# Performance work log

Measured on AMD Instinct MI355X. Metric: run time of the kernel, lower is better.

The kernel has to match this reference:

```python
import jax, jax.numpy as jnp
import numpy as np

N_NODE = 50000
D = 64
N_HEADS = 8
N_LAYERS = 2
NEG = -1e9
PAD = 0
STDV = 1.0 / np.sqrt(D)


def _l2norm(x, axis):
    n = jnp.sqrt(jnp.sum(x * x, axis=axis, keepdims=True))
    return x / jnp.maximum(n, 1e-12)


def _hgconv(x, theta, bias, edge_index):
    # PyG HypergraphConv (use_attention=False): out = D^-1 H B^-1 H^T (x @ theta) + bias
    xt = x @ theta
    node, hedge = edge_index[0], edge_index[1]
    ones = jnp.ones(node.shape[0], x.dtype)
    Bdeg = jax.ops.segment_sum(ones, hedge, num_segments=N_NODE)   # hyperedge degree
    Ddeg = jax.ops.segment_sum(ones, node, num_segments=N_NODE)    # node degree
    m = jax.ops.segment_sum(xt[node], hedge, num_segments=N_NODE)  # nodes -> hyperedges
    m = m * jnp.where(Bdeg > 0, 1.0 / Bdeg, 0.0)[:, None]
    out = jax.ops.segment_sum(m[hedge], node, num_segments=N_NODE) # hyperedges -> nodes
    out = out * jnp.where(Ddeg > 0, 1.0 / Ddeg, 0.0)[:, None]
    return out + bias


def _mha(x, w, pad_mask, reverse):
    # w: [4, D, D] -> q, k, v, out projections. reverse=True attends to future (triu).
    B, L, d = x.shape
    dk = d // N_HEADS
    split = lambda h: h.reshape(B, L, N_HEADS, dk).transpose(0, 2, 1, 3)
    q, k, v = split(x @ w[0]), split(x @ w[1]), split(x @ w[2])
    scores = jnp.einsum('bhid,bhjd->bhij', q, k) / jnp.sqrt(jnp.asarray(dk, x.dtype))
    tri = jnp.triu(jnp.ones((L, L), bool)) if reverse else jnp.tril(jnp.ones((L, L), bool))
    scores = jnp.where(tri[None, None], scores, NEG)
    scores = jnp.where(pad_mask[:, None, None, :], NEG, scores)
    attn = jax.nn.softmax(scores, axis=-1)
    out = jnp.einsum('bhij,bhjd->bhid', attn, v).transpose(0, 2, 1, 3).reshape(B, L, d)
    return out @ w[3], attn


def _prev_user_mask(seq):
    # scatter -1000 at every user id already seen up to position i (index 0 = PAD column)
    B, L = seq.shape
    tril = jnp.tril(jnp.ones((L, L), bool))
    idx = jnp.where(tril[None], seq[:, None, :], 0)                       # [B,L,L]
    idx = jnp.concatenate([idx, jnp.zeros((B, L, 1), idx.dtype)], axis=2)  # [B,L,L+1]
    b = jnp.arange(B)[:, None, None]
    i = jnp.arange(L)[None, :, None]
    return jnp.zeros((B, L, N_NODE), jnp.float32).at[b, i, idx].set(-1000.0)


def _hg_user(emb_table, gate_w, gate_b, att, att_m, theta, theta_b, edges):
    chans = []
    for c in range(3):
        x = emb_table * jax.nn.sigmoid(emb_table @ gate_w[c] + gate_b[c])  # self-gating
        acc, cur = x, x
        for k in range(N_LAYERS):
            cur = _hgconv(cur, theta[k], theta_b[k], edges[c])
            acc = acc + _l2norm(cur, axis=1)
        chans.append(acc / (N_LAYERS + 1))  # mean over [input, layer1, layer2]
    logits = jnp.stack([jnp.sum(att * (c @ att_m), axis=1) for c in chans], axis=1)  # [N,3]
    score = jax.nn.softmax(logits, axis=-1)
    return sum(score[:, i:i + 1] * chans[i] for i in range(3))


def setup_inputs() -> dict:
    key = jax.random.key(0)
    ks = jax.random.split(key, 20)
    u = lambda k, shp: jax.random.uniform(k, shp, jnp.float32, -STDV, STDV)
    B, L, E = 16, 50, 800000
    return {
        'input_seq': jax.random.randint(ks[0], (B, L), 0, N_NODE),
        'label_seq': jax.random.randint(ks[1], (B, L), 0, N_NODE),
        'input_time': jax.random.randint(ks[2], (B, L), 0, 100000),
        'label_time': jax.random.randint(ks[3], (B, L), 0, 100000),
        'edge_index_g': jax.random.randint(ks[4], (2, E), 0, N_NODE),
        'edge_index_i': jax.random.randint(ks[5], (2, E), 0, N_NODE),
        'edge_index_u': jax.random.randint(ks[6], (2, E), 0, N_NODE),
        'emb_table': u(ks[7], (N_NODE, D)),
        'gate_w': u(ks[8], (3, D, D)),
        'gate_b': u(ks[9], (3, D)),
        'att': u(ks[10], (D,)),
        'att_m': u(ks[11], (D, D)),
        'theta': u(ks[12], (N_LAYERS, D, D)),
        'theta_b': u(ks[13], (N_LAYERS, D)),
        'w_hist': u(ks[14], (4, D, D)),
        'w_fut': u(ks[15], (4, D, D)),
    }


def reference(input_seq, label_seq, input_time, label_time,
              edge_index_g, edge_index_i, edge_index_u,
              emb_table, gate_w, gate_b, att, att_m, theta, theta_b, w_hist, w_fut):
    # input_time / label_time are accepted but unused, as in the original forward.
    HG = _hg_user(emb_table, gate_w, gate_b, att, att_m, theta, theta_b,
                  (edge_index_g, edge_index_i, edge_index_u))
    pad_in = input_seq == PAD
    pad_lb = label_seq == PAD
    past_att_out, past_dist = _mha(HG[input_seq], w_hist, pad_in, reverse=False)
    fut_att_out, fut_dist = _mha(HG[label_seq], w_fut, pad_lb, reverse=True)
    output_past = (past_att_out @ HG.T + _prev_user_mask(input_seq)).reshape(-1, N_NODE)
    future_output = (fut_att_out @ HG.T).reshape(-1, N_NODE)
    return (output_past, future_output, past_dist, fut_dist,
            _l2norm(past_att_out, axis=1), _l2norm(fut_att_out, axis=1))
```

## Files before the change

### kernel.cpp

```cpp
#include <hip/hip_runtime.h>
#include <math.h>

#define N_NODE 50000
#define DD 64
#define NE 800000
#define BB 16
#define LL 50
#define NH 8
#define DK 8
#define NEGV -1e9f
#define NB 49
#define NBLK 256
#define EPB 3125

#define OFF_PDIST 80000000u
#define OFF_FDIST 80320000u
#define OFF_L2P 80640000u
#define OFF_L2F 80691200u

typedef unsigned short ushortt;
typedef __attribute__((ext_vector_type(8))) short bf16x8v;
typedef __attribute__((ext_vector_type(4))) float f32x4v;

__device__ __forceinline__ float b2f(ushortt h) { return __uint_as_float(((unsigned)h) << 16); }
__device__ __forceinline__ ushortt f2b(float f) {
    unsigned u = __float_as_uint(f);
    return (ushortt)((u + 0x7fffu + ((u >> 16) & 1u)) >> 16);
}
__device__ __forceinline__ void acc8(float* a, uint4 x) {
    a[0] += b2f((ushortt)(x.x)); a[1] += b2f((ushortt)(x.x >> 16));
    a[2] += b2f((ushortt)(x.y)); a[3] += b2f((ushortt)(x.y >> 16));
    a[4] += b2f((ushortt)(x.z)); a[5] += b2f((ushortt)(x.z >> 16));
    a[6] += b2f((ushortt)(x.w)); a[7] += b2f((ushortt)(x.w >> 16));
}
__device__ __forceinline__ uint4 pack8(const float* a) {
    uint4 w;
    w.x = (unsigned)f2b(a[0]) | ((unsigned)f2b(a[1]) << 16);
    w.y = (unsigned)f2b(a[2]) | ((unsigned)f2b(a[3]) << 16);
    w.z = (unsigned)f2b(a[4]) | ((unsigned)f2b(a[5]) << 16);
    w.w = (unsigned)f2b(a[6]) | ((unsigned)f2b(a[7]) << 16);
    return w;
}

__global__ void k_zero(float* p, int n) {
    int i = blockIdx.x * 256 + threadIdx.x;
    if (i < n) p[i] = 0.0f;
}

__global__ __launch_bounds__(256) void k_cnt(const int* __restrict__ eg,
                                             const int* __restrict__ ei,
                                             const int* __restrict__ eu,
                                             int* __restrict__ hist) {
    int c = blockIdx.y;
    const int* ed = (c == 0) ? eg : ((c == 1) ? ei : eu);
    int blk = blockIdx.x;
    __shared__ int lc[2 * NB];
    int tid = threadIdx.x;
    for (int j = tid; j < 2 * NB; j += 256) lc[j] = 0;
    __syncthreads();
    int e0 = blk * EPB;
    for (int i = e0 + tid; i < e0 + EPB; i += 256) {
        atomicAdd(&lc[ed[NE + i] >> 10], 1);
        atomicAdd(&lc[NB + (ed[i] >> 10)], 1);
    }
    __syncthreads();
    for (int j = tid; j < 2 * NB; j += 256) {
        int side = (j >= NB);
        int b = side ? (j - NB) : j;
        hist[(((side * 3 + c) * NB) + b) * NBLK + blk] = lc[j];
    }
}

__global__ __launch_bounds__(256) void k_scanH(int* __restrict__ hist, int* __restrict__ bb) {
    int t6 = blockIdx.x;
    int* h = hist + t6 * NB * NBLK;
    __shared__ int part[256];
    int tid = threadIdx.x;
    const int CH = (NB * NBLK) / 256;
    int base = tid * CH;
    int s = 0;
    for (int i = 0; i < CH; i++) s += h[base + i];
    part[tid] = s;
    __syncthreads();
    for (int o = 1; o < 256; o <<= 1) {
        int v = (tid >= o) ? part[tid - o] : 0;
        __syncthreads();
        part[tid] += v;
        __syncthreads();
    }
    int run = (tid == 0) ? 0 : part[tid - 1];
    for (int i = 0; i < CH; i++) {
        int idx = base + i;
        int v = h[idx];
        if ((idx & (NBLK - 1)) == 0) bb[t6 * (NB + 1) + (idx >> 8)] = run;
        h[idx] = run;
        run += v;
    }
    if (tid == 255) bb[t6 * (NB + 1) + NB] = run;
}

__global__ __launch_bounds__(256) void k_part2(const int* __restrict__ eg,
                                               const int* __restrict__ ei,
                                               const int* __restrict__ eu,
                                               const int* __restrict__ hist,
                                               unsigned* __restrict__ poolB,
                                               unsigned* __restrict__ poolD) {
    int c = blockIdx.y;
    const int* ed = (c == 0) ? eg : ((c == 1) ? ei : eu);
    int blk = blockIdx.x;
    __shared__ int curB[NB], curD[NB];
    int tid = threadIdx.x;
    for (int j = tid; j < NB; j += 256) {
        curB[j] = hist[(((0 * 3 + c) * NB) + j) * NBLK + blk];
        curD[j] = hist[(((1 * 3 + c) * NB) + j) * NBLK + blk];
    }
    __syncthreads();
    unsigned* pB = poolB + c * 800000;
    unsigned* pD = poolD + c * 800000;
    int e0 = blk * EPB;
    for (int i = e0 + tid; i < e0 + EPB; i += 256) {
        int n = ed[i], h = ed[NE + i];
        int pb = atomicAdd(&curB[h >> 10], 1);
        pB[pb] = ((unsigned)h << 16) | (unsigned)n;
        int pd = atomicAdd(&curD[n >> 10], 1);
        pD[pd] = ((unsigned)n << 16) | (unsigned)h;
    }
}

__global__ __launch_bounds__(256) void k_bucket(const unsigned* __restrict__ poolB,
                                                const unsigned* __restrict__ poolD,
                                                const int* __restrict__ bb,
                                                int* __restrict__ nbrB3, int* __restrict__ nbrD3,
                                                int* __restrict__ offB3, int* __restrict__ offD3,
                                                float* __restrict__ invB3, float* __restrict__ invD3) {
    int b = blockIdx.x, c = blockIdx.y, side = blockIdx.z;
    const unsigned* pool = (side ? poolD : poolB) + c * 800000;
    int* nbr = (side ? nbrD3 : nbrB3) + c * 800000;
    int* off = (side ? offD3 : offB3) + c * 50001;
    float* inv = (side ? invD3 : invB3) + c * 50000;
    int t6 = side * 3 + c;
    int s0 = bb[t6 * (NB + 1) + b], s1 = bb[t6 * (NB + 1) + b + 1];
    int baseSeg = b << 10;
    __shared__ int cnt[1024];
    __shared__ int ofs[1024];
    __shared__ int part[256];
    int tid = threadIdx.x;
    for (int j = tid; j < 1024; j += 256) cnt[j] = 0;
    __syncthreads();
    for (int i = s0 + tid; i < s1; i += 256)
        atomicAdd(&cnt[(pool[i] >> 16) & 1023], 1);
    __syncthreads();
    int t4 = tid * 4;
    int a0 = cnt[t4], a1 = cnt[t4 + 1], a2 = cnt[t4 + 2], a3 = cnt[t4 + 3];
    part[tid] = a0 + a1 + a2 + a3;
    __syncthreads();
    for (int o = 1; o < 256; o <<= 1) {
        int v = (tid >= o) ? part[tid - o] : 0;
        __syncthreads();
        part[tid] += v;
        __syncthreads();
    }
    int excl = (tid == 0) ? 0 : part[tid - 1];
    ofs[t4] = excl;
    ofs[t4 + 1] = excl + a0;
    ofs[t4 + 2] = excl + a0 + a1;
    ofs[t4 + 3] = excl + a0 + a1 + a2;
    __syncthreads();
    for (int ls = tid; ls < 1024; ls += 256) {
        int seg = baseSeg + ls;
        if (seg < N_NODE) {
            off[seg] = s0 + ofs[ls];
            inv[seg] = cnt[ls] ? 1.0f / (float)cnt[ls] : 0.0f;
        }
    }
    if (b == NB - 1 && tid == 0) off[N_NODE] = NE;
    __syncthreads();
    for (int i = s0 + tid; i < s1; i += 256) {
        unsigned u = pool[i];
        int ls = (u >> 16) & 1023;
        int p = atomicAdd(&ofs[ls], 1);
        nbr[s0 + p] = (int)(u & 0xFFFFu);
    }
}

__global__ __launch_bounds__(256) void k_gateX(const float* __restrict__ emb,
                                               const float* __restrict__ gate_w,
                                               const float* __restrict__ gate_b,
                                               float* __restrict__ acc3,
                                               ushortt* __restrict__ xt3) {
    int c = blockIdx.y;
    const float* W = gate_w + c * 4096;
    const float* bias = gate_b + c * 64;
    float* acc = acc3 + (size_t)c * 3200000;
    ushortt* xt = xt3 + (size_t)c * 3200000;
    __shared__ float sW[64 * 64];
    __shared__ float sx[4][64];
    int tid = threadIdx.x;
    for (int i = tid; i < 4096; i += 256) sW[i] = W[i];
    int r = tid >> 6;
    int d = tid & 63;
    int n = blockIdx.x * 4 + r;
    sx[r][d] = emb[n * DD + d];
    __syncthreads();
    float a = bias[d];
#pragma unroll
    for (int k = 0; k < 64; k++) a += sx[r][k] * sW[k * 64 + d];
    float x = sx[r][d] * (1.0f / (1.0f + expf(-a)));
    acc[n * DD + d] = x;
    xt[n * DD + d] = f2b(x);
}

__global__ __launch_bounds__(256) void k_gathB3(const ushortt* __restrict__ xt3,
                                                const int* __restrict__ offB3,
                                                const int* __restrict__ nbrB3,
                                                const float* __restrict__ invB3,
                                                ushortt* __restrict__ m3) {
    int c = blockIdx.y;
    const ushortt* src = xt3 + (size_t)c * 3200000;
    const int* off = offB3 + c * 50001;
    const int* nbr = nbrB3 + c * 800000;
    const float* invSeg = invB3 + c * 50000;
    ushortt* dst = m3 + (size_t)c * 3200000;
    int seg = blockIdx.x * 4 + (threadIdx.x >> 6);
    int lane = threadIdx.x & 63;
    int sub = lane >> 3;
    int c8 = lane & 7;
    int s = off[seg], e = off[seg + 1];
    float a[8] = {0.f, 0.f, 0.f, 0.f, 0.f, 0.f, 0.f, 0.f};
    int i = s + sub;
    if (i < e) {
        uint4 x = ((const uint4*)(src + (size_t)nbr[i] * DD))[c8];
        for (i += 8; i < e; i += 8) {
            uint4 nx = ((const uint4*)(src + (size_t)nbr[i] * DD))[c8];
            acc8(a, x);
            x = nx;
        }
        acc8(a, x);
    }
#pragma unroll
    for (int j = 0; j < 8; j++) {
        a[j] += __shfl_xor(a[j], 8, 64);
        a[j] += __shfl_xor(a[j], 16, 64);
        a[j] += __shfl_xor(a[j], 32, 64);
    }
    if (sub == 0) {
        float sc = invSeg[seg];
        float b[8];
#pragma unroll
        for (int j = 0; j < 8; j++) b[j] = a[j] * sc;
        ((uint4*)(dst + (size_t)seg * DD))[c8] = pack8(b);
    }
}

template <int WRITE_XT>
__global__ __launch_bounds__(256) void k_gathD3f(const ushortt* __restrict__ m3,
                                                 const int* __restrict__ offD3,
                                                 const int* __restrict__ nbrD3,
                                                 const float* __restrict__ invD3,
                                                 const float* __restrict__ theta,
                                                 const float* __restrict__ theta_b,
                                                 float* __restrict__ acc3,
                                                 ushortt* __restrict__ xt3) {
    int c = blockIdx.y;
    const ushortt* m = m3 + (size_t)c * 3200000;
    const int* off = offD3 + c * 50001;
    const int* nbr = nbrD3 + c * 800000;
    const float* invD = invD3 + c * 50000;
    float* acc = acc3 + (size_t)c * 3200000;
    ushortt* xt = xt3 + (size_t)c * 3200000;

    __shared__ float sTh[64 * 64];
    __shared__ float sx[4][64];
    __shared__ float sb[64];
    int tid = threadIdx.x;
    for (int i = tid; i < 4096; i += 256) sTh[i] = theta[i];
    if (tid < 64) sb[tid] = theta_b[tid];

    int w = tid >> 6;
    int seg = blockIdx.x * 4 + w;
    int lane = tid & 63;
    int sub = lane >> 3;
    int c8 = lane & 7;
    int s = off[seg], e = off[seg + 1];
    float a[8] = {0.f, 0.f, 0.f, 0.f, 0.f, 0.f, 0.f, 0.f};
    int i = s + sub;
    if (i < e) {
        uint4 x = ((const uint4*)(m + (size_t)nbr[i] * DD))[c8];
        for (i += 8; i < e; i += 8) {
            uint4 nx = ((const uint4*)(m + (size_t)nbr[i] * DD))[c8];
            acc8(a, x);
            x = nx;
        }
        acc8(a, x);
    }
#pragma unroll
    for (int j = 0; j < 8; j++) {
        a[j] += __shfl_xor(a[j], 8, 64);
        a[j] += __shfl_xor(a[j], 16, 64);
        a[j] += __shfl_xor(a[j], 32, 64);
    }
    if (sub == 0) {
        float iD = invD[seg];
#pragma unroll
        for (int j = 0; j < 8; j++) sx[w][c8 * 8 + j] = a[j] * iD;
    }
    __syncthreads();

    int d = lane;
    float v = sb[d];
#pragma unroll
    for (int k = 0; k < 64; k++) v += sx[w][k] * sTh[k * 64 + d];
    float ss = v * v;
#pragma unroll
    for (int o = 32; o; o >>= 1) ss += __shfl_xor(ss, o, 64);
    float nr = fmaxf(sqrtf(ss), 1e-12f);
    size_t idx = (size_t)seg * DD + d;
    acc[idx] += v / nr;
    if (WRITE_XT) xt[idx] = f2b(v);
}

__global__ __launch_bounds__(256) void k_comb(const float* __restrict__ a0,
                                              const float* __restrict__ a1,
                                              const float* __restrict__ a2,
                                              const float* __restrict__ att_m,
                                              const float* __restrict__ att,
                                              float* __restrict__ HG,
                                              ushortt* __restrict__ HG16) {
    __shared__ float svv[64];
    int tid = threadIdx.x;
    if (tid < 64) {
        float s = 0.f;
        for (int k = 0; k < 64; k++) s += att_m[tid * 64 + k] * att[k];
        svv[tid] = s;
    }
    __syncthreads();
    int r = tid >> 6;
    int d = tid & 63;
    int n = blockIdx.x * 4 + r;
    float x0 = a0[n * DD + d], x1 = a1[n * DD + d], x2 = a2[n * DD + d];
    float vd = svv[d];
    float l0 = x0 * vd, l1 = x1 * vd, l2 = x2 * vd;
#pragma unroll
    for (int o = 32; o; o >>= 1) {
        l0 += __shfl_xor(l0, o, 64);
        l1 += __shfl_xor(l1, o, 64);
        l2 += __shfl_xor(l2, o, 64);
    }
    l0 *= (1.0f / 3.0f); l1 *= (1.0f / 3.0f); l2 *= (1.0f / 3.0f);
    float mx = fmaxf(l0, fmaxf(l1, l2));
    float e0 = expf(l0 - mx), e1 = expf(l1 - mx), e2 = expf(l2 - mx);
    float inv = 1.0f / (e0 + e1 + e2);
    float hv = (e0 * x0 + e1 * x1 + e2 * x2) * inv * (1.0f / 3.0f);
    HG[n * DD + d] = hv;
    HG16[n * DD + d] = f2b(hv);
}

__global__ __launch_bounds__(256) void k_attn(const float* __restrict__ HG,
                                              const int* __restrict__ iseq,
                                              const int* __restrict__ lseq,
                                              const float* __restrict__ w_hist,
                                              const float* __restrict__ w_fut,
                                              float* __restrict__ dout,
                                              ushortt* __restrict__ attout16,
                                              float* __restrict__ attoutF) {
    int b = blockIdx.x;
    int dir = blockIdx.y;
    const int* seq = (dir == 0) ? iseq : lseq;
    const float* W = (dir == 0) ? w_hist : w_fut;
    float* dist = dout + ((dir == 0) ? OFF_PDIST : OFF_FDIST);

    __shared__ float sX[LL * 64];
    __shared__ float sQ[LL * 64];
    __shared__ float sK[LL * 64];
    __shared__ float sV[LL * 64];
    __shared__ float sS[LL * LL];
    __shared__ float sInv[64];
    __shared__ int sseq[LL];

    int tid = threadIdx.x;
    int w = tid >> 6;
    int lane = tid & 63;
    if (tid < LL) sseq[tid] = seq[b * LL + tid];
    __syncthreads();
    for (int idx = tid; idx < LL * 64; idx += 256) {
        int i = idx >> 6, d = idx & 63;
        sX[idx] = HG[sseq[i] * DD + d];
    }
    __syncthreads();
    for (int idx = tid; idx < LL * 64; idx += 256) {
        int i = idx >> 6, d = idx & 63;
        float q = 0, k = 0, v = 0;
        for (int kk = 0; kk < 64; kk++) {
            float x = sX[i * 64 + kk];
            q += x * W[kk * 64 + d];
            k += x * W[4096 + kk * 64 + d];
            v += x * W[8192 + kk * 64 + d];
        }
        sQ[idx] = q; sK[idx] = k; sV[idx] = v;
    }
    __syncthreads();
    for (int idx = tid; idx < LL * 64; idx += 256) sX[idx] = 0.0f;
    __syncthreads();

    const float scale = 0.35355339059327373f;
    for (int h = 0; h < NH; h++) {
        for (int idx = tid; idx < LL * LL; idx += 256) {
            int i = idx / LL, j = idx % LL;
            float s = 0;
#pragma unroll
            for (int d = 0; d < DK; d++) s += sQ[i * 64 + h * 8 + d] * sK[j * 64 + h * 8 + d];
            s *= scale;
            bool allowed = (dir == 0) ? (j <= i) : (j >= i);
            if (!allowed) s = NEGV;
            if (sseq[j] == 0) s = NEGV;
            sS[idx] = s;
        }
        __syncthreads();
        for (int i = w; i < LL; i += 4) {
            float v = (lane < LL) ? sS[i * LL + lane] : -INFINITY;
            float mx = v;
#pragma unroll
            for (int o = 32; o; o >>= 1) mx = fmaxf(mx, __shfl_xor(mx, o, 64));
            float e = (lane < LL) ? expf(v - mx) : 0.0f;
            float sum = e;
#pragma unroll
            for (int o = 32; o; o >>= 1) sum += __shfl_xor(sum, o, 64);
            float p = e / sum;
            if (lane < LL) {
                sS[i * LL + lane] = p;
                dist[((b * NH + h) * LL + i) * LL + lane] = p;
            }
        }
        __syncthreads();
        for (int idx = tid; idx < LL * DK; idx += 256) {
            int i = idx / DK, d8 = idx % DK;
            float o = 0;
            for (int j = 0; j < LL; j++) o += sS[i * LL + j] * sV[j * 64 + h * 8 + d8];
            sX[i * 64 + h * 8 + d8] = o;
        }
        __syncthreads();
    }
    for (int idx = tid; idx < LL * 64; idx += 256) {
        int i = idx >> 6, d = idx & 63;
        float o = 0;
        for (int kk = 0; kk < 64; kk++) o += sX[i * 64 + kk] * W[3 * 4096 + kk * 64 + d];
        sQ[idx] = o;
        int row = dir * 800 + b * LL + i;
        attout16[row * 64 + d] = f2b(o);
        if (attoutF) attoutF[row * 64 + d] = o;
    }
    __syncthreads();
    if (tid < 64) {
        float s = 0;
        for (int l = 0; l < LL; l++) {
            float x = sQ[l * 64 + tid];
            s += x * x;
        }
        sInv[tid] = 1.0f / fmaxf(sqrtf(s), 1e-12f);
    }
    __syncthreads();
    float* ol2 = dout + ((dir == 0) ? OFF_L2P : OFF_L2F) + b * LL * 64;
    for (int idx = tid; idx < LL * 64; idx += 256) {
        int d = idx & 63;
        ol2[idx] = sQ[idx] * sInv[d];
    }
}

__global__ __launch_bounds__(256) void k_bigmm_mfma(const ushortt* __restrict__ A16,
                                                    const ushortt* __restrict__ HG16,
                                                    float* __restrict__ out) {
    __shared__ float sO[16][260];
    int tid = threadIdx.x;
    int lane = tid & 63;
    int w = tid >> 6;
    int rt = blockIdx.y;
    int colBase = blockIdx.x * 256;
    int lrow = lane & 15;
    int kb = (lane >> 4) * 8;
    int arow = rt * 16 + lrow;
    bf16x8v a0 = *(const bf16x8v*)(A16 + (size_t)arow * 64 + kb);
    bf16x8v a1 = *(const bf16x8v*)(A16 + (size_t)arow * 64 + kb + 32);
#pragma unroll
    for (int ct = 0; ct < 4; ct++) {
        int lc = w * 64 + ct * 16 + lrow;
        int col = colBase + lc;
        int colc = (col < N_NODE) ? col : 0;
        bf16x8v b0 = *(const bf16x8v*)(HG16 + (size_t)colc * 64 + kb);
        bf16x8v b1 = *(const bf16x8v*)(HG16 + (size_t)colc * 64 + kb + 32);
        f32x4v acc = {0.f, 0.f, 0.f, 0.f};
        acc = __builtin_amdgcn_mfma_f32_16x16x32_bf16(a0, b0, acc, 0, 0, 0);
        acc = __builtin_amdgcn_mfma_f32_16x16x32_bf16(a1, b1, acc, 0, 0, 0);
        int r0 = (lane >> 4) * 4;
#pragma unroll
        for (int j = 0; j < 4; j++) sO[r0 + j][lc] = acc[j];
    }
    __syncthreads();
#pragma unroll
    for (int j = 0; j < 4; j++) {
        int r = w * 4 + j;
        int row = rt * 16 + r;
        int c0 = colBase + lane * 4;
        f32x4v v = {sO[r][lane * 4], sO[r][lane * 4 + 1],
                    sO[r][lane * 4 + 2], sO[r][lane * 4 + 3]};
        if (c0 + 3 < N_NODE) {
            __builtin_nontemporal_store(v, (f32x4v*)(out + (size_t)row * 50000 + c0));
        } else {
            for (int t = 0; t < 4; t++)
                if (c0 + t < N_NODE) out[(size_t)row * 50000 + c0 + t] = v[t];
        }
    }
}

__global__ __launch_bounds__(64) void k_mask(const int* __restrict__ iseq,
                                             float* __restrict__ out) {
    int row = blockIdx.x;
    int b = row / LL, i = row % LL;
    __shared__ int s[LL];
    int tid = threadIdx.x;
    if (tid < LL) s[tid] = iseq[b * LL + tid];
    __syncthreads();
    float* o = out + (size_t)row * 50000;
    if (tid == 0) o[0] -= 1000.0f;
    if (tid < LL && tid <= i) {
        int c = s[tid];
        if (c > 0 && c < N_NODE) {
            bool first = true;
            for (int j = 0; j < tid; j++)
                if (s[j] == c) { first = false; break; }
            if (first) o[c] -= 1000.0f;
        }
    }
}

__global__ void k_deg(const int* __restrict__ node, const int* __restrict__ hedge,
                      float* __restrict__ Ddeg, float* __restrict__ Bdeg) {
    int e = blockIdx.x * 256 + threadIdx.x;
    if (e < NE) {
        atomicAdd(&Ddeg[node[e]], 1.0f);
        atomicAdd(&Bdeg[hedge[e]], 1.0f);
    }
}

__global__ void k_inv(float* a, int n) {
    int i = blockIdx.x * 256 + threadIdx.x;
    if (i < n) a[i] = (a[i] > 0.0f) ? (1.0f / a[i]) : 0.0f;
}

__global__ __launch_bounds__(256) void k_scat(const float* __restrict__ src,
                                              const int* __restrict__ gidx,
                                              const int* __restrict__ sidx,
                                              const float* __restrict__ scale,
                                              float* __restrict__ dst) {
    int e = blockIdx.x * 4 + (threadIdx.x >> 6);
    int d = threadIdx.x & 63;
    if (e >= NE) return;
    int g = gidx[e];
    int s = sidx[e];
    float v = src[g * DD + d];
    if (scale) v *= scale[g];
    atomicAdd(&dst[s * DD + d], v);
}

__global__ __launch_bounds__(256) void k_fin(float* __restrict__ cur,
                                             const float* __restrict__ invD,
                                             const float* __restrict__ bias,
                                             float* __restrict__ acc) {
    int r = threadIdx.x >> 6;
    int d = threadIdx.x & 63;
    int n = blockIdx.x * 4 + r;
    float v = cur[n * DD + d] * invD[n] + bias[d];
    cur[n * DD + d] = v;
    float s = v * v;
#pragma unroll
    for (int o = 32; o; o >>= 1) s += __shfl_xor(s, o, 64);
    float nr = fmaxf(sqrtf(s), 1e-12f);
    acc[n * DD + d] += v / nr;
}

__global__ __launch_bounds__(256) void k_gate(const float* __restrict__ emb,
                                              const float* __restrict__ W,
                                              const float* __restrict__ bias,
                                              float* __restrict__ cur,
                                              float* __restrict__ acc) {
    __shared__ float sW[64 * 64];
    __shared__ float sx[4][64];
    int tid = threadIdx.x;
    for (int i = tid; i < 4096; i += 256) sW[i] = W[i];
    int r = tid >> 6;
    int d = tid & 63;
    int n = blockIdx.x * 4 + r;
    sx[r][d] = emb[n * DD + d];
    __syncthreads();
    float a = bias[d];
#pragma unroll
    for (int k = 0; k < 64; k++) a += sx[r][k] * sW[k * 64 + d];
    float x = sx[r][d] * (1.0f / (1.0f + expf(-a)));
    cur[n * DD + d] = x;
    acc[n * DD + d] = x;
}

__global__ __launch_bounds__(256) void k_mm64(const float* __restrict__ X,
                                              const float* __restrict__ W,
                                              float* __restrict__ Y) {
    __shared__ float sW[64 * 64];
    __shared__ float sx[4][64];
    int tid = threadIdx.x;
    for (int i = tid; i < 4096; i += 256) sW[i] = W[i];
    int r = tid >> 6;
    int d = tid & 63;
    int n = blockIdx.x * 4 + r;
    sx[r][d] = X[n * DD + d];
    __syncthreads();
    float a = 0.0f;
#pragma unroll
    for (int k = 0; k < 64; k++) a += sx[r][k] * sW[k * 64 + d];
    Y[n * DD + d] = a;
}

__global__ __launch_bounds__(256) void k_bigmm5(const float* __restrict__ A,
                                                const float* __restrict__ HG,
                                                float* __restrict__ out) {
    int col = blockIdx.x * 256 + threadIdx.x;
    int r0 = blockIdx.y * 400;
    bool ok = (col < N_NODE);
    float4 h[16];
    const float4* hp = (const float4*)(HG + (size_t)(ok ? col : 0) * 64);
#pragma unroll
    for (int t = 0; t < 16; t++) h[t] = hp[t];
    if (!ok) return;
    for (int r = 0; r < 400; r++) {
        int row = r0 + r;
        const float* ar = A + (size_t)row * 64;
        float q0 = 0.f, q1 = 0.f, q2 = 0.f, q3 = 0.f;
#pragma unroll
        for (int t = 0; t < 16; t++) {
            q0 += ar[4 * t + 0] * h[t].x;
            q1 += ar[4 * t + 1] * h[t].y;
            q2 += ar[4 * t + 2] * h[t].z;
            q3 += ar[4 * t + 3] * h[t].w;
        }
        out[(size_t)row * 50000 + col] = (q0 + q1) + (q2 + q3);
    }
}

extern "C" void kernel_launch(void* const* d_in, const int* in_sizes, int n_in,
                              void* d_out, int out_size, void* d_ws, size_t ws_size,
                              hipStream_t stream) {
    const int* input_seq = (const int*)d_in[0];
    const int* label_seq = (const int*)d_in[1];
    const int* eg = (const int*)d_in[4];
    const int* ei = (const int*)d_in[5];
    const int* eu = (const int*)d_in[6];
    const float* emb = (const float*)d_in[7];
    const float* gate_w = (const float*)d_in[8];
    const float* gate_b = (const float*)d_in[9];
    const float* att = (const float*)d_in[10];
    const float* att_m = (const float*)d_in[11];
    const float* theta = (const float*)d_in[12];
    const float* theta_b = (const float*)d_in[13];
    const float* w_hist = (const float*)d_in[14];
    const float* w_fut = (const float*)d_in[15];

    float* out = (float*)d_out;
    float* ws = (float*)d_ws;

    const size_t HGF = 3200000;
    const int HISTN = 6 * NB * NBLK;
    const size_t needA = (HGF + 150000 + 150000 +
                          (size_t)(HISTN + 6 * (NB + 1) + 64) +
                          300006 + 4 * 2400000 +
                          2 * 2400000 +
                          3 * HGF +
                          HGF / 2 + 51200 + 1024) * 4;

    if (ws_size >= needA) {
        size_t o = 0;
        float* HG = ws + o; o += HGF;
        float* invB3 = ws + o; o += 150000;
        float* invD3 = ws + o; o += 150000;
        int* hist = (int*)(ws + o); o += HISTN;
        int* bbarr = (int*)(ws + o); o += 6 * (NB + 1) + 64;
        int* offB3 = (int*)(ws + o); o += 150003;
        int* offD3 = (int*)(ws + o); o += 150003 + 2;
        int* nbrB3 = (int*)(ws + o); o += 2400000;
        int* nbrD3 = (int*)(ws + o); o += 2400000;
        unsigned* poolB = (unsigned*)(ws + o); o += 2400000;
        unsigned* poolD = (unsigned*)(ws + o); o += 2400000;
        ushortt* xt3 = (ushortt*)(ws + o); o += 4800000;
        ushortt* m3 = (ushortt*)(ws + o); o += 4800000;
        float* acc3 = ws + o; o += 3 * HGF;
        ushortt* HG16 = (ushortt*)(ws + o); o += HGF / 2;
        ushortt* A16 = (ushortt*)(ws + o); o += 51200;

        dim3 pg(NBLK, 3);
        k_cnt<<<pg, 256, 0, stream>>>(eg, ei, eu, hist);
        k_scanH<<<6, 256, 0, stream>>>(hist, bbarr);
        k_part2<<<pg, 256, 0, stream>>>(eg, ei, eu, hist, poolB, poolD);
        dim3 dg(NB, 3, 2);
        k_bucket<<<dg, 256, 0, stream>>>(poolB, poolD, bbarr, nbrB3, nbrD3,
                                         offB3, offD3, invB3, invD3);

        dim3 ng3(12500, 3);
        k_gateX<<<ng3, 256, 0, stream>>>(emb, gate_w, gate_b, acc3, xt3);
        k_gathB3<<<ng3, 256, 0, stream>>>(xt3, offB3, nbrB3, invB3, m3);
        k_gathD3f<1><<<ng3, 256, 0, stream>>>(m3, offD3, nbrD3, invD3,
                                              theta, theta_b, acc3, xt3);
        k_gathB3<<<ng3, 256, 0, stream>>>(xt3, offB3, nbrB3, invB3, m3);
        k_gathD3f<0><<<ng3, 256, 0, stream>>>(m3, offD3, nbrD3, invD3,
                                              theta + 4096, theta_b + 64, acc3, xt3);

        k_comb<<<12500, 256, 0, stream>>>(acc3, acc3 + HGF, acc3 + 2 * HGF,
                                          att_m, att, HG, HG16);
        dim3 ag(BB, 2);
        k_attn<<<ag, 256, 0, stream>>>(HG, input_seq, label_seq, w_hist, w_fut,
                                       out, A16, nullptr);
        dim3 bg(196, 100);
        k_bigmm_mfma<<<bg, 256, 0, stream>>>(A16, HG16, out);
        k_mask<<<BB * LL, 64, 0, stream>>>(input_seq, out);
    } else {
        float* HG = ws;
        float* invB = HG + HGF;
        float* invD = invB + 50000;
        if (ws_size < (HGF + 100000 + 64) * 4) {
            HG = out + 36550000u;
            invB = HG + HGF;
            invD = invB + 50000;
        }
        float* trans = out;
        float* acc0 = trans;
        float* acc1 = trans + HGF;
        float* acc2 = trans + 2 * HGF;
        float* cur = trans + 3 * HGF;
        float* xt = trans + 4 * HGF;
        float* m = trans + 5 * HGF;
        float* accs[3] = {acc0, acc1, acc2};
        const int* edges[3] = {eg, ei, eu};
        for (int c = 0; c < 3; c++) {
            const int* node = edges[c];
            const int* hedge = edges[c] + NE;
            k_zero<<<(100000 + 255) / 256, 256, 0, stream>>>(invB, 100000);
            k_deg<<<(NE + 255) / 256, 256, 0, stream>>>(node, hedge, invD, invB);
            k_inv<<<(100000 + 255) / 256, 256, 0, stream>>>(invB, 100000);
            k_gate<<<12500, 256, 0, stream>>>(emb, gate_w + c * 4096, gate_b + c * 64, cur, accs[c]);
            for (int k = 0; k < 2; k++) {
                k_mm64<<<12500, 256, 0, stream>>>(cur, theta + k * 4096, xt);
                k_zero<<<12500, 256, 0, stream>>>(m, (int)HGF);
                k_scat<<<NE / 4, 256, 0, stream>>>(xt, node, hedge, nullptr, m);
                k_zero<<<12500, 256, 0, stream>>>(cur, (int)HGF);
                k_scat<<<NE / 4, 256, 0, stream>>>(m, hedge, node, invB, cur);
                k_fin<<<12500, 256, 0, stream>>>(cur, invD, theta_b + k * 64, accs[c]);
            }
        }
        k_comb<<<12500, 256, 0, stream>>>(acc0, acc1, acc2, att_m, att, HG, (ushortt*)m);
        dim3 ag(BB, 2);
        k_attn<<<ag, 256, 0, stream>>>(HG, input_seq, label_seq, w_hist, w_fut,
                                       out, (ushortt*)(m + HGF), xt);
        dim3 bg5(196, 4);
        k_bigmm5<<<bg5, 256, 0, stream>>>(xt, HG, out);
        k_mask<<<BB * LL, 64, 0, stream>>>(input_seq, out);
    }
}
```

Baseline: 829.6 us.

## Split attention per head across blocks and remap gather blocks for XCD locality

The attention kernel used to run only 32 blocks and loop over the 8 heads one after another. It is now split into a per-head kernel on a (batch, head, dir) grid that writes per-head outputs to a workspace buffer, followed by a separate kernel for the output projection and L2 normalisation. The hypergraph gather kernels switch to a 1D grid whose block-id mapping pins each channel's blocks to a fixed subset of the XCDs (block id mod 8), aiming to keep each channel's data in its own L2. The extra workspace, kernel launch and global round-trip are the cost, and a slightly oversized grid has early-exiting blocks.

```diff
diff --git a/kernel.cpp b/kernel.cpp
--- a/kernel.cpp
+++ b/kernel.cpp
@@ -40,6 +40,14 @@
     w.z = (unsigned)f2b(a[4]) | ((unsigned)f2b(a[5]) << 16);
     w.w = (unsigned)f2b(a[6]) | ((unsigned)f2b(a[7]) << 16);
     return w;
+}
+__device__ __forceinline__ bool xcd_map(int bid, int& c, int& slot) {
+    int r = bid & 7;
+    c = (r * 3) >> 3;
+    int nclass = (c == 2) ? 2 : 3;
+    int base = (c == 0) ? 0 : ((c == 1) ? 3 : 6);
+    slot = (bid >> 3) * nclass + (r - base);
+    return slot < 12500;
 }
 
 __global__ void k_zero(float* p, int n) {
@@ -215,13 +223,14 @@
                                                 const int* __restrict__ nbrB3,
                                                 const float* __restrict__ invB3,
                                                 ushortt* __restrict__ m3) {
-    int c = blockIdx.y;
+    int c, slot;
+    if (!xcd_map(blockIdx.x, c, slot)) return;
     const ushortt* src = xt3 + (size_t)c * 3200000;
     const int* off = offB3 + c * 50001;
     const int* nbr = nbrB3 + c * 800000;
     const float* invSeg = invB3 + c * 50000;
     ushortt* dst = m3 + (size_t)c * 3200000;
-    int seg = blockIdx.x * 4 + (threadIdx.x >> 6);
+    int seg = slot * 4 + (threadIdx.x >> 6);
     int lane = threadIdx.x & 63;
     int sub = lane >> 3;
     int c8 = lane & 7;
@@ -261,7 +270,8 @@
                                                  const float* __restrict__ theta_b,
                                                  float* __restrict__ acc3,
                                                  ushortt* __restrict__ xt3) {
-    int c = blockIdx.y;
+    int c, slot;
+    if (!xcd_map(blockIdx.x, c, slot)) return;
     const ushortt* m = m3 + (size_t)c * 3200000;
     const int* off = offD3 + c * 50001;
     const int* nbr = nbrD3 + c * 800000;
@@ -277,7 +287,7 @@
     if (tid < 64) sb[tid] = theta_b[tid];
 
     int w = tid >> 6;
-    int seg = blockIdx.x * 4 + w;
+    int seg = slot * 4 + w;
     int lane = tid & 63;
     int sub = lane >> 3;
     int c8 = lane & 7;
@@ -355,115 +365,110 @@
     HG16[n * DD + d] = f2b(hv);
 }
 
-__global__ __launch_bounds__(256) void k_attn(const float* __restrict__ HG,
-                                              const int* __restrict__ iseq,
-                                              const int* __restrict__ lseq,
-                                              const float* __restrict__ w_hist,
-                                              const float* __restrict__ w_fut,
-                                              float* __restrict__ dout,
-                                              ushortt* __restrict__ attout16,
-                                              float* __restrict__ attoutF) {
-    int b = blockIdx.x;
-    int dir = blockIdx.y;
-    const int* seq = (dir == 0) ? iseq : lseq;
-    const float* W = (dir == 0) ? w_hist : w_fut;
-    float* dist = dout + ((dir == 0) ? OFF_PDIST : OFF_FDIST);
-
+__global__ __launch_bounds__(256) void k_attnh(const float* __restrict__ HG,
+                                               const int* __restrict__ iseq,
+                                               const int* __restrict__ lseq,
+                                               const float* __restrict__ w_hist,
+                                               const float* __restrict__ w_fut,
+                                               float* __restrict__ dout,
+                                               float* __restrict__ hout) {
+    int b = blockIdx.x, h = blockIdx.y, dir = blockIdx.z;
+    const int* seq = dir ? lseq : iseq;
+    const float* W = dir ? w_fut : w_hist;
+    float* dist = dout + (dir ? OFF_FDIST : OFF_PDIST);
     __shared__ float sX[LL * 64];
-    __shared__ float sQ[LL * 64];
-    __shared__ float sK[LL * 64];
-    __shared__ float sV[LL * 64];
+    __shared__ float sQ[LL * DK], sK[LL * DK], sV[LL * DK];
     __shared__ float sS[LL * LL];
-    __shared__ float sInv[64];
     __shared__ int sseq[LL];
-
-    int tid = threadIdx.x;
-    int w = tid >> 6;
-    int lane = tid & 63;
+    int tid = threadIdx.x, w = tid >> 6, lane = tid & 63;
     if (tid < LL) sseq[tid] = seq[b * LL + tid];
     __syncthreads();
-    for (int idx = tid; idx < LL * 64; idx += 256) {
-        int i = idx >> 6, d = idx & 63;
-        sX[idx] = HG[sseq[i] * DD + d];
-    }
-    __syncthreads();
-    for (int idx = tid; idx < LL * 64; idx += 256) {
-        int i = idx >> 6, d = idx & 63;
+    for (int idx = tid; idx < LL * 64; idx += 256)
+        sX[idx] = HG[sseq[idx >> 6] * DD + (idx & 63)];
+    __syncthreads();
+    for (int idx = tid; idx < LL * DK; idx += 256) {
+        int i = idx / DK, d = idx % DK;
+        int col = h * 8 + d;
         float q = 0, k = 0, v = 0;
         for (int kk = 0; kk < 64; kk++) {
             float x = sX[i * 64 + kk];
-            q += x * W[kk * 64 + d];
-            k += x * W[4096 + kk * 64 + d];
-            v += x * W[8192 + kk * 64 + d];
+            q += x * W[kk * 64 + col];
+            k += x * W[4096 + kk * 64 + col];
+            v += x * W[8192 + kk * 64 + col];
         }
         sQ[idx] = q; sK[idx] = k; sV[idx] = v;
     }
     __syncthreads();
-    for (int idx = tid; idx < LL * 64; idx += 256) sX[idx] = 0.0f;
-    __syncthreads();
-
     const float scale = 0.35355339059327373f;
-    for (int h = 0; h < NH; h++) {
-        for (int idx = tid; idx < LL * LL; idx += 256) {
-            int i = idx / LL, j = idx % LL;
-            float s = 0;
-#pragma unroll
-            for (int d = 0; d < DK; d++) s += sQ[i * 64 + h * 8 + d] * sK[j * 64 + h * 8 + d];
-            s *= scale;
-            bool allowed = (dir == 0) ? (j <= i) : (j >= i);
-            if (!allowed) s = NEGV;
-            if (sseq[j] == 0) s = NEGV;
-            sS[idx] = s;
-        }
-        __syncthreads();
-        for (int i = w; i < LL; i += 4) {
-            float v = (lane < LL) ? sS[i * LL + lane] : -INFINITY;
-            float mx = v;
-#pragma unroll
-            for (int o = 32; o; o >>= 1) mx = fmaxf(mx, __shfl_xor(mx, o, 64));
-            float e = (lane < LL) ? expf(v - mx) : 0.0f;
-            float sum = e;
-#pragma unroll
-            for (int o = 32; o; o >>= 1) sum += __shfl_xor(sum, o, 64);
-            float p = e / sum;
-            if (lane < LL) {
-                sS[i * LL + lane] = p;
-                dist[((b * NH + h) * LL + i) * LL + lane] = p;
-            }
-        }
-        __syncthreads();
-        for (int idx = tid; idx < LL * DK; idx += 256) {
-            int i = idx / DK, d8 = idx % DK;
-            float o = 0;
-            for (int j = 0; j < LL; j++) o += sS[i * LL + j] * sV[j * 64 + h * 8 + d8];
-            sX[i * 64 + h * 8 + d8] = o;
-        }
-        __syncthreads();
-    }
+    for (int idx = tid; idx < LL * LL; idx += 256) {
+        int i = idx / LL, j = idx % LL;
+        float s = 0;
+#pragma unroll
+        for (int d = 0; d < DK; d++) s += sQ[i * DK + d] * sK[j * DK + d];
+        s *= scale;
+        bool allowed = dir ? (j >= i) : (j <= i);
+        if (!allowed || sseq[j] == 0) s = NEGV;
+        sS[idx] = s;
+    }
+    __syncthreads();
+    for (int i = w; i < LL; i += 4) {
+        float v = (lane < LL) ? sS[i * LL + lane] : -INFINITY;
+        float mx = v;
+#pragma unroll
+        for (int o = 32; o; o >>= 1) mx = fmaxf(mx, __shfl_xor(mx, o, 64));
+        float e = (lane < LL) ? expf(v - mx) : 0.0f;
+        float sum = e;
+#pragma unroll
+        for (int o = 32; o; o >>= 1) sum += __shfl_xor(sum, o, 64);
+        float p = e / sum;
+        if (lane < LL) {
+            sS[i * LL + lane] = p;
+            dist[((b * NH + h) * LL + i) * LL + lane] = p;
+        }
+    }
+    __syncthreads();
+    for (int idx = tid; idx < LL * DK; idx += 256) {
+        int i = idx / DK, d = idx % DK;
+        float o = 0;
+        for (int j = 0; j < LL; j++) o += sS[i * LL + j] * sV[j * DK + d];
+        hout[((size_t)(dir * 800 + b * LL + i)) * 64 + h * 8 + d] = o;
+    }
+}
+
+__global__ __launch_bounds__(256) void k_attno(const float* __restrict__ hout,
+                                               const float* __restrict__ w_hist,
+                                               const float* __restrict__ w_fut,
+                                               float* __restrict__ dout,
+                                               ushortt* __restrict__ attout16) {
+    int b = blockIdx.x, dir = blockIdx.y;
+    const float* W = dir ? w_fut : w_hist;
+    __shared__ float sH[LL * 64];
+    __shared__ float sO[LL * 64];
+    __shared__ float sInv[64];
+    int tid = threadIdx.x;
+    for (int idx = tid; idx < LL * 64; idx += 256)
+        sH[idx] = hout[((size_t)(dir * 800 + b * LL)) * 64 + idx];
+    __syncthreads();
     for (int idx = tid; idx < LL * 64; idx += 256) {
         int i = idx >> 6, d = idx & 63;
         float o = 0;
-        for (int kk = 0; kk < 64; kk++) o += sX[i * 64 + kk] * W[3 * 4096 + kk * 64 + d];
-        sQ[idx] = o;
+        for (int kk = 0; kk < 64; kk++) o += sH[i * 64 + kk] * W[3 * 4096 + kk * 64 + d];
+        sO[idx] = o;
         int row = dir * 800 + b * LL + i;
         attout16[row * 64 + d] = f2b(o);
-        if (attoutF) attoutF[row * 64 + d] = o;
     }
     __syncthreads();
     if (tid < 64) {
         float s = 0;
         for (int l = 0; l < LL; l++) {
-            float x = sQ[l * 64 + tid];
+            float x = sO[l * 64 + tid];
             s += x * x;
         }
         sInv[tid] = 1.0f / fmaxf(sqrtf(s), 1e-12f);
     }
     __syncthreads();
-    float* ol2 = dout + ((dir == 0) ? OFF_L2P : OFF_L2F) + b * LL * 64;
-    for (int idx = tid; idx < LL * 64; idx += 256) {
-        int d = idx & 63;
-        ol2[idx] = sQ[idx] * sInv[d];
-    }
+    float* ol2 = dout + (dir ? OFF_L2F : OFF_L2P) + b * LL * 64;
+    for (int idx = tid; idx < LL * 64; idx += 256) ol2[idx] = sO[idx] * sInv[idx & 63];
 }
 
 __global__ __launch_bounds__(256) void k_bigmm_mfma(const ushortt* __restrict__ A16,
@@ -615,6 +620,109 @@
 #pragma unroll
     for (int k = 0; k < 64; k++) a += sx[r][k] * sW[k * 64 + d];
     Y[n * DD + d] = a;
+}
+
+__global__ __launch_bounds__(256) void k_attnF(const float* __restrict__ HG,
+                                               const int* __restrict__ iseq,
+                                               const int* __restrict__ lseq,
+                                               const float* __restrict__ w_hist,
+                                               const float* __restrict__ w_fut,
+                                               float* __restrict__ dout,
+                                               float* __restrict__ attoutF) {
+    int b = blockIdx.x;
+    int dir = blockIdx.y;
+    const int* seq = (dir == 0) ? iseq : lseq;
+    const float* W = (dir == 0) ? w_hist : w_fut;
+    float* dist = dout + ((dir == 0) ? OFF_PDIST : OFF_FDIST);
+    __shared__ float sX[LL * 64];
+    __shared__ float sQ[LL * 64];
+    __shared__ float sK[LL * 64];
+    __shared__ float sV[LL * 64];
+    __shared__ float sS[LL * LL];
+    __shared__ float sInv[64];
+    __shared__ int sseq[LL];
+    int tid = threadIdx.x;
+    int w = tid >> 6, lane = tid & 63;
+    if (tid < LL) sseq[tid] = seq[b * LL + tid];
+    __syncthreads();
+    for (int idx = tid; idx < LL * 64; idx += 256) {
+        int i = idx >> 6, d = idx & 63;
+        sX[idx] = HG[sseq[i] * DD + d];
+    }
+    __syncthreads();
+    for (int idx = tid; idx < LL * 64; idx += 256) {
+        int i = idx >> 6, d = idx & 63;
+        float q = 0, k = 0, v = 0;
+        for (int kk = 0; kk < 64; kk++) {
+            float x = sX[i * 64 + kk];
+            q += x * W[kk * 64 + d];
+            k += x * W[4096 + kk * 64 + d];
+            v += x * W[8192 + kk * 64 + d];
+        }
+        sQ[idx] = q; sK[idx] = k; sV[idx] = v;
+    }
+    __syncthreads();
+    for (int idx = tid; idx < LL * 64; idx += 256) sX[idx] = 0.0f;
+    __syncthreads();
+    const float scale = 0.35355339059327373f;
+    for (int h = 0; h < NH; h++) {
+        for (int idx = tid; idx < LL * LL; idx += 256) {
+            int i = idx / LL, j = idx % LL;
+            float s = 0;
+#pragma unroll
+            for (int d = 0; d < DK; d++) s += sQ[i * 64 + h * 8 + d] * sK[j * 64 + h * 8 + d];
+            s *= scale;
+            bool allowed = (dir == 0) ? (j <= i) : (j >= i);
+            if (!allowed || sseq[j] == 0) s = NEGV;
+            sS[idx] = s;
+        }
+        __syncthreads();
+        for (int i = w; i < LL; i += 4) {
+            float v = (lane < LL) ? sS[i * LL + lane] : -INFINITY;
+            float mx = v;
+#pragma unroll
+            for (int o = 32; o; o >>= 1) mx = fmaxf(mx, __shfl_xor(mx, o, 64));
+            float e = (lane < LL) ? expf(v - mx) : 0.0f;
+            float sum = e;
+#pragma unroll
+            for (int o = 32; o; o >>= 1) sum += __shfl_xor(sum, o, 64);
+            float p = e / sum;
+            if (lane < LL) {
+                sS[i * LL + lane] = p;
+                dist[((b * NH + h) * LL + i) * LL + lane] = p;
+            }
+        }
+        __syncthreads();
+        for (int idx = tid; idx < LL * DK; idx += 256) {
+            int i = idx / DK, d8 = idx % DK;
+            float o = 0;
+            for (int j = 0; j < LL; j++) o += sS[i * LL + j] * sV[j * 64 + h * 8 + d8];
+            sX[i * 64 + h * 8 + d8] = o;
+        }
+        __syncthreads();
+    }
+    for (int idx = tid; idx < LL * 64; idx += 256) {
+        int i = idx >> 6, d = idx & 63;
+        float o = 0;
+        for (int kk = 0; kk < 64; kk++) o += sX[i * 64 + kk] * W[3 * 4096 + kk * 64 + d];
+        sQ[idx] = o;
+        attoutF[(dir * 800 + b * LL + i) * 64 + d] = o;
+    }
+    __syncthreads();
+    if (tid < 64) {
+        float s = 0;
+        for (int l = 0; l < LL; l++) {
+            float x = sQ[l * 64 + tid];
+            s += x * x;
+        }
+        sInv[tid] = 1.0f / fmaxf(sqrtf(s), 1e-12f);
+    }
+    __syncthreads();
+    float* ol2 = dout + ((dir == 0) ? OFF_L2P : OFF_L2F) + b * LL * 64;
+    for (int idx = tid; idx < LL * 64; idx += 256) {
+        int d = idx & 63;
+        ol2[idx] = sQ[idx] * sInv[d];
+    }
 }
 
 __global__ __launch_bounds__(256) void k_bigmm5(const float* __restrict__ A,
@@ -671,7 +779,7 @@
                           300006 + 4 * 2400000 +
                           2 * 2400000 +
                           3 * HGF +
-                          HGF / 2 + 51200 + 1024) * 4;
+                          HGF / 2 + 51200 + 102400 + 1024) * 4;
 
     if (ws_size >= needA) {
         size_t o = 0;
@@ -691,6 +799,7 @@
         float* acc3 = ws + o; o += 3 * HGF;
         ushortt* HG16 = (ushortt*)(ws + o); o += HGF / 2;
         ushortt* A16 = (ushortt*)(ws + o); o += 51200;
+        float* hout = ws + o; o += 102400;
 
         dim3 pg(NBLK, 3);
         k_cnt<<<pg, 256, 0, stream>>>(eg, ei, eu, hist);
@@ -702,18 +811,19 @@
 
         dim3 ng3(12500, 3);
         k_gateX<<<ng3, 256, 0, stream>>>(emb, gate_w, gate_b, acc3, xt3);
-        k_gathB3<<<ng3, 256, 0, stream>>>(xt3, offB3, nbrB3, invB3, m3);
-        k_gathD3f<1><<<ng3, 256, 0, stream>>>(m3, offD3, nbrD3, invD3,
-                                              theta, theta_b, acc3, xt3);
-        k_gathB3<<<ng3, 256, 0, stream>>>(xt3, offB3, nbrB3, invB3, m3);
-        k_gathD3f<0><<<ng3, 256, 0, stream>>>(m3, offD3, nbrD3, invD3,
-                                              theta + 4096, theta_b + 64, acc3, xt3);
+        k_gathB3<<<50000, 256, 0, stream>>>(xt3, offB3, nbrB3, invB3, m3);
+        k_gathD3f<1><<<50000, 256, 0, stream>>>(m3, offD3, nbrD3, invD3,
+                                                theta, theta_b, acc3, xt3);
+        k_gathB3<<<50000, 256, 0, stream>>>(xt3, offB3, nbrB3, invB3, m3);
+        k_gathD3f<0><<<50000, 256, 0, stream>>>(m3, offD3, nbrD3, invD3,
+                                                theta + 4096, theta_b + 64, acc3, xt3);
 
         k_comb<<<12500, 256, 0, stream>>>(acc3, acc3 + HGF, acc3 + 2 * HGF,
                                           att_m, att, HG, HG16);
-        dim3 ag(BB, 2);
-        k_attn<<<ag, 256, 0, stream>>>(HG, input_seq, label_seq, w_hist, w_fut,
-                                       out, A16, nullptr);
+        dim3 ah(BB, NH, 2);
+        k_attnh<<<ah, 256, 0, stream>>>(HG, input_seq, label_seq, w_hist, w_fut, out, hout);
+        dim3 ao(BB, 2);
+        k_attno<<<ao, 256, 0, stream>>>(hout, w_hist, w_fut, out, A16);
         dim3 bg(196, 100);
         k_bigmm_mfma<<<bg, 256, 0, stream>>>(A16, HG16, out);
         k_mask<<<BB * LL, 64, 0, stream>>>(input_seq, out);
@@ -753,8 +863,7 @@
         }
         k_comb<<<12500, 256, 0, stream>>>(acc0, acc1, acc2, att_m, att, HG, (ushortt*)m);
         dim3 ag(BB, 2);
-        k_attn<<<ag, 256, 0, stream>>>(HG, input_seq, label_seq, w_hist, w_fut,
-                                       out, (ushortt*)(m + HGF), xt);
+        k_attnF<<<ag, 256, 0, stream>>>(HG, input_seq, label_seq, w_hist, w_fut, out, xt);
         dim3 bg5(196, 4);
         k_bigmm5<<<bg5, 256, 0, stream>>>(xt, HG, out);
         k_mask<<<BB * LL, 64, 0, stream>>>(input_seq, out);
```

Measured after the change: 867.0 us. 1.05x slower.
